# Kernel optimization log

Measured on AMD Instinct MI355X. Metric: run time of the kernel, lower is better.

The kernel has to match this reference:

```python
import jax, jax.numpy as jnp
import numpy as np

N_NODES = 10000
N_EDGES = 120000
F_IN = 66
HEADS = 10
F_HEAD = 66          # GATConv(66, 66, heads=10) -> concat 660
GCN_OUT = F_IN * HEADS * 2  # 1320


def leaky(x, slope):
    return jnp.where(x >= 0, x, slope * x)


def add_self_loops(edge_index, n):
    loops = jnp.arange(n, dtype=edge_index.dtype)
    src = jnp.concatenate([edge_index[0], loops])
    dst = jnp.concatenate([edge_index[1], loops])
    return src, dst


def gat_conv(x, src, dst, W, att_src, att_dst, bias, n):
    # x: [N, F_IN]; W: [F_IN, HEADS*F_HEAD]
    xt = (x @ W).reshape(n, HEADS, F_HEAD)
    a_s = jnp.sum(xt * att_src, axis=-1)   # [N, H]
    a_d = jnp.sum(xt * att_dst, axis=-1)   # [N, H]
    e = leaky(a_s[src] + a_d[dst], 0.2)    # [E, H]
    # segment softmax over destination nodes
    m = jax.ops.segment_max(e, dst, num_segments=n)
    m = jnp.where(jnp.isfinite(m), m, 0.0)
    ex = jnp.exp(e - m[dst])
    s = jax.ops.segment_sum(ex, dst, num_segments=n)
    alpha = ex / jnp.maximum(s[dst], 1e-16)        # [E, H]
    msg = xt[src] * alpha[:, :, None]              # [E, H, F_HEAD]
    out = jax.ops.segment_sum(msg, dst, num_segments=n)
    return out.reshape(n, HEADS * F_HEAD) + bias


def gcn_conv(x, src, dst, W, b, n):
    xt = x @ W                                     # [N, GCN_OUT]
    ones = jnp.ones(src.shape[0], dtype=xt.dtype)
    deg = jax.ops.segment_sum(ones, dst, num_segments=n)
    dinv = jax.lax.rsqrt(jnp.maximum(deg, 1.0))
    norm = dinv[src] * dinv[dst]                   # [E]
    out = jax.ops.segment_sum(xt[src] * norm[:, None], dst, num_segments=n)
    return out + b


def setup_inputs() -> dict:
    key = jax.random.key(0)
    ks = jax.random.split(key, 16)
    x = jax.random.normal(ks[0], (N_NODES, F_IN), dtype=jnp.float32)
    edge_index = jax.random.randint(ks[1], (2, N_EDGES), 0, N_NODES, dtype=jnp.int32)
    sc = 0.05
    p = {
        'x': x,
        'edge_index': edge_index,
        'W_gat': jax.random.normal(ks[2], (F_IN, HEADS * F_HEAD)) * sc,
        'att_src': jax.random.normal(ks[3], (HEADS, F_HEAD)) * sc,
        'att_dst': jax.random.normal(ks[4], (HEADS, F_HEAD)) * sc,
        'b_gat': jnp.zeros((HEADS * F_HEAD,), jnp.float32),
        'W_gcn': jax.random.normal(ks[5], (HEADS * F_HEAD, GCN_OUT)) * sc,
        'b_gcn': jnp.zeros((GCN_OUT,), jnp.float32),
        'W_g1': jax.random.normal(ks[6], (GCN_OUT, 1000)) * sc,
        'b_g1': jnp.zeros((1000,), jnp.float32),
        'W_g2': jax.random.normal(ks[7], (1000, 64)) * sc,
        'b_g2': jnp.zeros((64,), jnp.float32),
        'W_fc1': jax.random.normal(ks[8], (64, 32)) * sc,
        'b_fc1': jnp.zeros((32,), jnp.float32),
        'W_fc2': jax.random.normal(ks[9], (32, 16)) * sc,
        'b_fc2': jnp.zeros((16,), jnp.float32),
        'W_out': jax.random.normal(ks[10], (16, 1)) * sc,
        'b_out': jnp.zeros((1,), jnp.float32),
    }
    return p


def reference(x, edge_index, W_gat, att_src, att_dst, b_gat, W_gcn, b_gcn,
              W_g1, b_g1, W_g2, b_g2, W_fc1, b_fc1, W_fc2, b_fc2, W_out, b_out):
    n = x.shape[0]
    src, dst = add_self_loops(edge_index, n)
    h = gat_conv(x, src, dst, W_gat, att_src, att_dst, b_gat, n)
    h = leaky(h, 0.01)
    h = gcn_conv(h, src, dst, W_gcn, b_gcn, n)
    h = leaky(h, 0.01)
    h = leaky(h @ W_g1 + b_g1, 0.01)   # dropout = identity (eval)
    h = h @ W_g2 + b_g2
    h = leaky(h, 0.01)
    h = leaky(h @ W_fc1 + b_fc1, 0.01)
    h = leaky(h @ W_fc2 + b_fc2, 0.01)
    return h @ W_out + b_out
```

## Files before the change

kernel.cpp:

```cpp
#include <hip/hip_runtime.h>
#include <hip/hip_bf16.h>
#include <math.h>

#define N_NODES 10000
#define MPAD    10112
#define N_EDGESI 120000
#define E_TOT   130000
#define F_INPUT 66
#define HEADS   10
#define F_HEAD  66
#define F_GAT   660
#define F_GCN   1320
#define F_G1    1000
#define F_G2    64

typedef _Float16 half_t;
typedef __attribute__((ext_vector_type(4))) _Float16 f16x4;
typedef __attribute__((ext_vector_type(8))) _Float16 f16x8;
typedef __attribute__((ext_vector_type(4))) float f32x4;

#define KP_GAT 128
#define NP_GAT 768
#define KP_GCN 704
#define NP_GCN 1408
#define KP_G1  1344
#define NP_G1  1024
#define KP_G2  1024
#define NP_G2  128

__device__ __forceinline__ float lky(float x, float s){ return x >= 0.f ? x : s*x; }

#if defined(__has_builtin)
#if __has_builtin(__builtin_amdgcn_global_load_lds)
#define HAVE_GLL 1
#endif
#endif

#ifdef HAVE_GLL
#define LDSLOAD16(g, l) __builtin_amdgcn_global_load_lds( \
    (const __attribute__((address_space(1))) void*)(g),   \
    (__attribute__((address_space(3))) void*)(l), 16, 0, 0)
#else
#define LDSLOAD16(g, l) (*(f16x8*)(l) = *(const f16x8*)(g))
#endif


__global__ void k_count(const int* __restrict__ ei, int* __restrict__ counts){
    int e = blockIdx.x*256 + threadIdx.x;
    if (e >= E_TOT) return;
    int dst = (e < N_EDGESI) ? ei[N_EDGESI + e] : (e - N_EDGESI);
    atomicAdd(&counts[dst], 1);
}

__global__ void k_scan(const int* __restrict__ counts, int* __restrict__ offsets){
    __shared__ int sh[256];
    int carry = 0;
    for (int base = 0; base < N_NODES; base += 256){
        int i = base + threadIdx.x;
        int v = (i < N_NODES) ? counts[i] : 0;
        sh[threadIdx.x] = v;
        __syncthreads();
        for (int off = 1; off < 256; off <<= 1){
            int t = (threadIdx.x >= off) ? sh[threadIdx.x - off] : 0;
            __syncthreads();
            sh[threadIdx.x] += t;
            __syncthreads();
        }
        if (i < N_NODES) offsets[i] = carry + sh[threadIdx.x] - v;
        int tot = sh[255];
        __syncthreads();
        carry += tot;
    }
    if (threadIdx.x == 0) offsets[N_NODES] = carry;
}

__global__ void k_fill(const int* __restrict__ ei, const int* __restrict__ offsets,
                       int* __restrict__ cursor, int* __restrict__ src_sorted){
    int e = blockIdx.x*256 + threadIdx.x;
    if (e >= E_TOT) return;
    int s, d;
    if (e < N_EDGESI){ s = ei[e]; d = ei[N_EDGESI + e]; }
    else { s = e - N_EDGESI; d = s; }
    int pos = offsets[d] + atomicAdd(&cursor[d], 1);
    src_sorted[pos] = s;
}


__global__ void k_xh(const float* __restrict__ x, half_t* __restrict__ xh){
    int idx = blockIdx.x*256 + threadIdx.x;
    if (idx >= MPAD*KP_GAT) return;
    int r = idx >> 7, c = idx & 127;
    float v = (r < N_NODES && c < F_INPUT) ? x[r*F_INPUT + c] : 0.f;
    xh[idx] = (half_t)v;
}

__global__ void k_wt(const float* __restrict__ W, half_t* __restrict__ WT,
                     int K, int N, int Kp, int Np){
    int idx = blockIdx.x*256 + threadIdx.x;
    if (idx >= Np*Kp) return;
    int n = idx / Kp, k = idx - n*Kp;
    float v = (n < N && k < K) ? W[(size_t)k*N + n] : 0.f;
    WT[idx] = (half_t)v;
}

__global__ __launch_bounds__(256)
void k_hgemm(const half_t* __restrict__ A, const half_t* __restrict__ Bt,
             half_t* __restrict__ C, const float* __restrict__ bias,
             int Nreal, int ldc, int Kp, float slope){
    __shared__ half_t As[128*64];
    __shared__ half_t Bs[128*64];
    const int tid = threadIdx.x;
    const int l = tid & 63;
    const int wid = tid >> 6;
    const int wr = wid >> 1, wc = wid & 1;
    const int brow = blockIdx.y * 128;
    const int bcol = blockIdx.x * 128;

    f32x4 acc[4][4] = {};

    for (int k0 = 0; k0 < Kp; k0 += 64){
        #pragma unroll
        for (int i = 0; i < 4; i++){
            int s = tid + i*256;
            int row = s >> 3, chp = s & 7;
            int ch = chp ^ (row & 7);
            LDSLOAD16(A  + (size_t)(brow+row)*Kp + k0 + ch*8, &As[s*8]);
            LDSLOAD16(Bt + (size_t)(bcol+row)*Kp + k0 + ch*8, &Bs[s*8]);
        }
        __syncthreads();
        #pragma unroll
        for (int t = 0; t < 2; t++){
            f16x8 af[4], bf[4];
            #pragma unroll
            for (int m = 0; m < 4; m++){
                int row = wr*64 + m*16 + (l & 15);
                int ch = (t*4 + (l >> 4)) ^ (row & 7);
                af[m] = *(const f16x8*)&As[row*64 + ch*8];
            }
            #pragma unroll
            for (int n = 0; n < 4; n++){
                int row = wc*64 + n*16 + (l & 15);
                int ch = (t*4 + (l >> 4)) ^ (row & 7);
                bf[n] = *(const f16x8*)&Bs[row*64 + ch*8];
            }
            #pragma unroll
            for (int m = 0; m < 4; m++)
                #pragma unroll
                for (int n = 0; n < 4; n++)
                    acc[m][n] = __builtin_amdgcn_mfma_f32_16x16x32_f16(
                        af[m], bf[n], acc[m][n], 0, 0, 0);
        }
        __syncthreads();
    }

    #pragma unroll
    for (int m = 0; m < 4; m++){
        #pragma unroll
        for (int n = 0; n < 4; n++){
            int col = bcol + wc*64 + n*16 + (l & 15);
            if (col >= ldc) continue;
            float bv = (bias && col < Nreal) ? bias[col] : 0.f;
            #pragma unroll
            for (int r = 0; r < 4; r++){
                int rowg = brow + wr*64 + m*16 + ((l >> 4) << 2) + r;
                float v = (col < Nreal) ? acc[m][n][r] + bv : 0.f;
                v = (v >= 0.f) ? v : slope*v;
                C[(size_t)rowg*ldc + col] = (half_t)v;
            }
        }
    }
}


__global__ void k_attn_ad(const half_t* __restrict__ xt,
                          const float* __restrict__ att_src, const float* __restrict__ att_dst,
                          float* __restrict__ a_s, float* __restrict__ a_d){
    int t = blockIdx.x*256 + threadIdx.x;
    if (t >= N_NODES*HEADS) return;
    int n = t / HEADS, h = t - (t/HEADS)*HEADS;
    const half_t* xr = xt + (size_t)n*NP_GAT + h*F_HEAD;
    const float* as = att_src + h*F_HEAD;
    const float* ad = att_dst + h*F_HEAD;
    float s = 0.f, d = 0.f;
    for (int f = 0; f < F_HEAD; f++){ float v = (float)xr[f]; s += v*as[f]; d += v*ad[f]; }
    a_s[t] = s; a_d[t] = d;
}

__global__ void k_softmax(const int* __restrict__ offsets, const int* __restrict__ src_sorted,
                          const float* __restrict__ a_s, const float* __restrict__ a_d,
                          float* __restrict__ e_sorted, float* __restrict__ inv_s){
    int t = blockIdx.x*256 + threadIdx.x;
    if (t >= N_NODES*HEADS) return;
    int n = t / HEADS, h = t - (t/HEADS)*HEADS;
    int b = offsets[n], e = offsets[n+1];
    float ad_n = a_d[t - h + h];
    ad_n = a_d[t];
    float m = -INFINITY;
    for (int s = b; s < e; s++){
        float v = lky(a_s[src_sorted[s]*HEADS + h] + ad_n, 0.2f);
        e_sorted[(size_t)s*HEADS + h] = v;
        m = fmaxf(m, v);
    }
    float sum = 0.f;
    for (int s = b; s < e; s++){
        float ex = __expf(e_sorted[(size_t)s*HEADS + h] - m);
        e_sorted[(size_t)s*HEADS + h] = ex;
        sum += ex;
    }
    inv_s[t] = 1.0f / fmaxf(sum, 1e-16f);
}

__global__ __launch_bounds__(192)
void k_gat_agg(const int* __restrict__ offsets, const int* __restrict__ src_sorted,
               const float* __restrict__ e_sorted, const float* __restrict__ inv_s,
               const half_t* __restrict__ xt, const float* __restrict__ b_gat,
               half_t* __restrict__ out){
    int n = blockIdx.x, t = threadIdx.x;
    int f0 = 4*t;
    int h0 = min(f0/F_HEAD, HEADS-1);
    int h1 = min((f0+1)/F_HEAD, HEADS-1);
    int h2 = min((f0+2)/F_HEAD, HEADS-1);
    int h3 = min((f0+3)/F_HEAD, HEADS-1);
    int b = offsets[n], e = offsets[n+1];
    float a0=0.f, a1=0.f, a2=0.f, a3=0.f;
    int s = b;
    for (; s + 2 <= e; s += 2){
        int s0 = src_sorted[s], s1 = src_sorted[s+1];
        f16x4 v0 = *(const f16x4*)(xt + (size_t)s0*NP_GAT + f0);
        f16x4 v1 = *(const f16x4*)(xt + (size_t)s1*NP_GAT + f0);
        const float* e0 = e_sorted + (size_t)s*HEADS;
        const float* e1 = e0 + HEADS;
        a0 += e0[h0]*(float)v0.x + e1[h0]*(float)v1.x;
        a1 += e0[h1]*(float)v0.y + e1[h1]*(float)v1.y;
        a2 += e0[h2]*(float)v0.z + e1[h2]*(float)v1.z;
        a3 += e0[h3]*(float)v0.w + e1[h3]*(float)v1.w;
    }
    if (s < e){
        int s0 = src_sorted[s];
        f16x4 v0 = *(const f16x4*)(xt + (size_t)s0*NP_GAT + f0);
        const float* e0 = e_sorted + (size_t)s*HEADS;
        a0 += e0[h0]*(float)v0.x;
        a1 += e0[h1]*(float)v0.y;
        a2 += e0[h2]*(float)v0.z;
        a3 += e0[h3]*(float)v0.w;
    }
    if (f0 >= KP_GCN) return;
    half_t* orow = out + (size_t)n*KP_GCN + f0;
    if (f0 < F_GAT){
        const float* iv = inv_s + n*HEADS;
        f16x4 r;
        r.x = (half_t)lky(a0*iv[h0] + b_gat[f0  ], 0.01f);
        r.y = (half_t)lky(a1*iv[h1] + b_gat[f0+1], 0.01f);
        r.z = (half_t)lky(a2*iv[h2] + b_gat[f0+2], 0.01f);
        r.w = (half_t)lky(a3*iv[h3] + b_gat[f0+3], 0.01f);
        *(f16x4*)orow = r;
    } else {
        f16x4 z = {(half_t)0.f,(half_t)0.f,(half_t)0.f,(half_t)0.f};
        *(f16x4*)orow = z;
    }
}


__global__ void k_dinv(const int* __restrict__ offsets, float* __restrict__ dinv){
    int n = blockIdx.x*256 + threadIdx.x;
    if (n >= N_NODES) return;
    float deg = (float)(offsets[n+1] - offsets[n]);
    dinv[n] = rsqrtf(fmaxf(deg, 1.0f));
}

__global__ __launch_bounds__(192)
void k_gcn_pre(const int* __restrict__ offsets, const int* __restrict__ src_sorted,
               const float* __restrict__ dinv, const half_t* __restrict__ h1,
               half_t* __restrict__ agg){
    int n = blockIdx.x, t = threadIdx.x;
    if (t >= 176) return;
    int f0 = 4*t;
    int b = offsets[n], e = offsets[n+1];
    float a0=0.f, a1=0.f, a2=0.f, a3=0.f;
    int s = b;
    for (; s + 2 <= e; s += 2){
        int s0 = src_sorted[s], s1 = src_sorted[s+1];
        float n0 = dinv[s0], n1 = dinv[s1];
        f16x4 v0 = *(const f16x4*)(h1 + (size_t)s0*KP_GCN + f0);
        f16x4 v1 = *(const f16x4*)(h1 + (size_t)s1*KP_GCN + f0);
        a0 += n0*(float)v0.x + n1*(float)v1.x;
        a1 += n0*(float)v0.y + n1*(float)v1.y;
        a2 += n0*(float)v0.z + n1*(float)v1.z;
        a3 += n0*(float)v0.w + n1*(float)v1.w;
    }
    if (s < e){
        int s0 = src_sorted[s];
        float n0 = dinv[s0];
        f16x4 v0 = *(const f16x4*)(h1 + (size_t)s0*KP_GCN + f0);
        a0 += n0*(float)v0.x;
        a1 += n0*(float)v0.y;
        a2 += n0*(float)v0.z;
        a3 += n0*(float)v0.w;
    }
    float dn = dinv[n];
    f16x4 r;
    r.x = (half_t)(dn*a0); r.y = (half_t)(dn*a1);
    r.z = (half_t)(dn*a2); r.w = (half_t)(dn*a3);
    *(f16x4*)(agg + (size_t)n*KP_GCN + f0) = r;
}

__global__ __launch_bounds__(256)
void k_tail(const half_t* __restrict__ h4,
            const float* __restrict__ Wfc1, const float* __restrict__ bfc1,
            const float* __restrict__ Wfc2, const float* __restrict__ bfc2,
            const float* __restrict__ Wout, const float* __restrict__ bout,
            float* __restrict__ out){
    __shared__ float W1[64*32];
    __shared__ float W2[32*16];
    __shared__ float Wo[16];
    __shared__ float b1[32];
    __shared__ float b2[16];
    __shared__ float r1[8][32];
    __shared__ float r2[8][16];
    int tid = threadIdx.x;
    for (int i = tid; i < 64*32; i += 256) W1[i] = Wfc1[i];
    for (int i = tid; i < 32*16; i += 256) W2[i] = Wfc2[i];
    if (tid < 16) Wo[tid] = Wout[tid];
    if (tid < 32) b1[tid] = bfc1[tid];
    if (tid < 16) b2[tid] = bfc2[tid];
    __syncthreads();
    int g = tid >> 5, j = tid & 31;
    int node = blockIdx.x*8 + g;
    const half_t* hr = h4 + (size_t)node*F_G2;
    float acc = 0.f;
    #pragma unroll 8
    for (int i = 0; i < 64; i++) acc += (float)hr[i]*W1[i*32 + j];
    r1[g][j] = lky(acc + b1[j], 0.01f);
    __syncthreads();
    if (j < 16){
        float a2 = 0.f;
        #pragma unroll
        for (int i = 0; i < 32; i++) a2 += r1[g][i]*W2[i*16 + j];
        r2[g][j] = lky(a2 + b2[j], 0.01f);
    }
    __syncthreads();
    if (j == 0){
        float a3 = 0.f;
        #pragma unroll
        for (int i = 0; i < 16; i++) a3 += r2[g][i]*Wo[i];
        out[node] = a3 + bout[0];
    }
}


extern "C" void kernel_launch(void* const* d_in, const int* in_sizes, int n_in,
                              void* d_out, int out_size, void* d_ws, size_t ws_size,
                              hipStream_t stream){
    const float* x       = (const float*)d_in[0];
    const int*   ei      = (const int*)  d_in[1];
    const float* W_gat   = (const float*)d_in[2];
    const float* att_src = (const float*)d_in[3];
    const float* att_dst = (const float*)d_in[4];
    const float* b_gat   = (const float*)d_in[5];
    const float* W_gcn   = (const float*)d_in[6];
    const float* b_gcn   = (const float*)d_in[7];
    const float* W_g1    = (const float*)d_in[8];
    const float* b_g1    = (const float*)d_in[9];
    const float* W_g2    = (const float*)d_in[10];
    const float* b_g2    = (const float*)d_in[11];
    const float* W_fc1   = (const float*)d_in[12];
    const float* b_fc1   = (const float*)d_in[13];
    const float* W_fc2   = (const float*)d_in[14];
    const float* b_fc2   = (const float*)d_in[15];
    const float* W_out   = (const float*)d_in[16];
    const float* b_out   = (const float*)d_in[17];
    float* out = (float*)d_out;
    char* ws = (char*)d_ws;

    size_t off = 0;
    auto alloc = [&](size_t bytes){ size_t o = off; off += (bytes + 255) & ~(size_t)255; return o; };
    size_t o_counts = alloc(N_NODES*4);
    size_t o_cursor = alloc(N_NODES*4);
    size_t o_offs   = alloc((N_NODES+1)*4);
    size_t o_as     = alloc(N_NODES*HEADS*4);
    size_t o_ad     = alloc(N_NODES*HEADS*4);
    size_t o_invs   = alloc(N_NODES*HEADS*4);
    size_t o_dinv   = alloc(N_NODES*4);
    size_t o_srcs   = alloc(E_TOT*4);
    size_t o_esrt   = alloc((size_t)E_TOT*HEADS*4);
    size_t o_xh     = alloc((size_t)MPAD*KP_GAT*2);
    size_t o_xt     = alloc((size_t)MPAD*NP_GAT*2);
    size_t o_h1     = alloc((size_t)N_NODES*KP_GCN*2);
    size_t o_agg    = alloc((size_t)MPAD*KP_GCN*2);
    size_t o_h2     = alloc((size_t)MPAD*KP_G1*2);
    size_t o_h3     = alloc((size_t)MPAD*KP_G2*2);
    size_t o_h4     = alloc((size_t)MPAD*F_G2*2);
    size_t o_wgatT  = alloc((size_t)NP_GAT*KP_GAT*2);
    size_t o_wgcnT  = alloc((size_t)NP_GCN*KP_GCN*2);
    size_t o_wg1T   = alloc((size_t)NP_G1*KP_G1*2);
    size_t o_wg2T   = alloc((size_t)NP_G2*KP_G2*2);

    int*    counts  = (int*)(ws + o_counts);
    int*    cursor  = (int*)(ws + o_cursor);
    int*    offsets = (int*)(ws + o_offs);
    float*  a_s     = (float*)(ws + o_as);
    float*  a_d     = (float*)(ws + o_ad);
    float*  inv_s   = (float*)(ws + o_invs);
    float*  dinv    = (float*)(ws + o_dinv);
    int*    src_srt = (int*)(ws + o_srcs);
    float*  e_srt   = (float*)(ws + o_esrt);
    half_t* xh      = (half_t*)(ws + o_xh);
    half_t* xt_h    = (half_t*)(ws + o_xt);
    half_t* h1h     = (half_t*)(ws + o_h1);
    half_t* aggh    = (half_t*)(ws + o_agg);
    half_t* h2h     = (half_t*)(ws + o_h2);
    half_t* h3h     = (half_t*)(ws + o_h3);
    half_t* h4h     = (half_t*)(ws + o_h4);
    half_t* WgatT   = (half_t*)(ws + o_wgatT);
    half_t* WgcnT   = (half_t*)(ws + o_wgcnT);
    half_t* Wg1T    = (half_t*)(ws + o_wg1T);
    half_t* Wg2T    = (half_t*)(ws + o_wg2T);

    hipMemsetAsync(counts, 0, N_NODES*4, stream);
    hipMemsetAsync(cursor, 0, N_NODES*4, stream);
    k_count<<<(E_TOT+255)/256, 256, 0, stream>>>(ei, counts);
    k_scan<<<1, 256, 0, stream>>>(counts, offsets);
    k_fill<<<(E_TOT+255)/256, 256, 0, stream>>>(ei, offsets, cursor, src_srt);
    k_dinv<<<(N_NODES+255)/256, 256, 0, stream>>>(offsets, dinv);

    k_xh<<<(MPAD*KP_GAT+255)/256, 256, 0, stream>>>(x, xh);
    k_wt<<<(NP_GAT*KP_GAT+255)/256, 256, 0, stream>>>(W_gat, WgatT, F_INPUT, F_GAT, KP_GAT, NP_GAT);
    k_wt<<<(NP_GCN*KP_GCN+255)/256, 256, 0, stream>>>(W_gcn, WgcnT, F_GAT, F_GCN, KP_GCN, NP_GCN);
    k_wt<<<(NP_G1*KP_G1+255)/256, 256, 0, stream>>>(W_g1, Wg1T, F_GCN, F_G1, KP_G1, NP_G1);
    k_wt<<<(NP_G2*KP_G2+255)/256, 256, 0, stream>>>(W_g2, Wg2T, F_G1, F_G2, KP_G2, NP_G2);

    k_hgemm<<<dim3(NP_GAT/128, MPAD/128), 256, 0, stream>>>(
        xh, WgatT, xt_h, nullptr, F_GAT, NP_GAT, KP_GAT, 1.0f);
    k_attn_ad<<<(N_NODES*HEADS+255)/256, 256, 0, stream>>>(xt_h, att_src, att_dst, a_s, a_d);
    k_softmax<<<(N_NODES*HEADS+255)/256, 256, 0, stream>>>(offsets, src_srt, a_s, a_d, e_srt, inv_s);
    k_gat_agg<<<N_NODES, 192, 0, stream>>>(offsets, src_srt, e_srt, inv_s, xt_h, b_gat, h1h);

    k_gcn_pre<<<N_NODES, 192, 0, stream>>>(offsets, src_srt, dinv, h1h, aggh);
    k_hgemm<<<dim3(NP_GCN/128, MPAD/128), 256, 0, stream>>>(
        aggh, WgcnT, h2h, b_gcn, F_GCN, KP_G1, KP_GCN, 0.01f);

    k_hgemm<<<dim3(NP_G1/128, MPAD/128), 256, 0, stream>>>(
        h2h, Wg1T, h3h, b_g1, F_G1, KP_G2, KP_G1, 0.01f);
    k_hgemm<<<dim3(NP_G2/128, MPAD/128), 256, 0, stream>>>(
        h3h, Wg2T, h4h, b_g2, F_G2, F_G2, KP_G2, 0.01f);
    k_tail<<<N_NODES/8, 256, 0, stream>>>(h4h, W_fc1, b_fc1, W_fc2, b_fc2,
                                          W_out, b_out, out);
}
```

Baseline: 386.0 us.

## Remap GEMM workgroups per XCD and unroll gather loops by four

The GEMM kernel now remaps its linear workgroup id so that neighbouring output tiles are placed on the same XCD, which should improve L2 reuse of the A and B panels on MI355X's multi-die layout. The GAT and GCN aggregation loops are unrolled from two to four neighbours per iteration, so more independent gather loads are in flight at once. The attention-coefficient kernel reads pairs of half values with unrolled loops, and a redundant a_d load is removed. The costs are higher register pressure in the aggregation kernels and a more complex tile-index computation.

```diff
diff --git a/kernel.cpp b/kernel.cpp
--- a/kernel.cpp
+++ b/kernel.cpp
@@ -15,6 +15,7 @@
 #define F_G2    64
 
 typedef _Float16 half_t;
+typedef __attribute__((ext_vector_type(2))) _Float16 f16x2;
 typedef __attribute__((ext_vector_type(4))) _Float16 f16x4;
 typedef __attribute__((ext_vector_type(8))) _Float16 f16x8;
 typedef __attribute__((ext_vector_type(4))) float f32x4;
@@ -113,8 +114,17 @@
     const int l = tid & 63;
     const int wid = tid >> 6;
     const int wr = wid >> 1, wc = wid & 1;
-    const int brow = blockIdx.y * 128;
-    const int bcol = blockIdx.x * 128;
+
+    const int gx = gridDim.x;
+    const int nwg = gx * gridDim.y;
+    const int orig = blockIdx.y * gx + blockIdx.x;
+    const int q = nwg >> 3, r8 = nwg & 7;
+    const int xcd = orig & 7, lin = orig >> 3;
+    const int wgid = (xcd < r8 ? xcd*(q+1) : r8*(q+1) + (xcd-r8)*q) + lin;
+    const int bx = wgid % gx, by = wgid / gx;
+
+    const int brow = by * 128;
+    const int bcol = bx * 128;
 
     f32x4 acc[4][4] = {};
 
@@ -182,7 +192,13 @@
     const float* as = att_src + h*F_HEAD;
     const float* ad = att_dst + h*F_HEAD;
     float s = 0.f, d = 0.f;
-    for (int f = 0; f < F_HEAD; f++){ float v = (float)xr[f]; s += v*as[f]; d += v*ad[f]; }
+    #pragma unroll
+    for (int f = 0; f < F_HEAD; f += 2){
+        f16x2 v = *(const f16x2*)(xr + f);
+        float vx = (float)v.x, vy = (float)v.y;
+        s += vx*as[f] + vy*as[f+1];
+        d += vx*ad[f] + vy*ad[f+1];
+    }
     a_s[t] = s; a_d[t] = d;
 }
 
@@ -193,8 +209,7 @@
     if (t >= N_NODES*HEADS) return;
     int n = t / HEADS, h = t - (t/HEADS)*HEADS;
     int b = offsets[n], e = offsets[n+1];
-    float ad_n = a_d[t - h + h];
-    ad_n = a_d[t];
+    float ad_n = a_d[t];
     float m = -INFINITY;
     for (int s = b; s < e; s++){
         float v = lky(a_s[src_sorted[s]*HEADS + h] + ad_n, 0.2f);
@@ -224,18 +239,23 @@
     int b = offsets[n], e = offsets[n+1];
     float a0=0.f, a1=0.f, a2=0.f, a3=0.f;
     int s = b;
-    for (; s + 2 <= e; s += 2){
-        int s0 = src_sorted[s], s1 = src_sorted[s+1];
+    for (; s + 4 <= e; s += 4){
+        int s0 = src_sorted[s],   s1 = src_sorted[s+1];
+        int s2 = src_sorted[s+2], s3 = src_sorted[s+3];
         f16x4 v0 = *(const f16x4*)(xt + (size_t)s0*NP_GAT + f0);
         f16x4 v1 = *(const f16x4*)(xt + (size_t)s1*NP_GAT + f0);
+        f16x4 v2 = *(const f16x4*)(xt + (size_t)s2*NP_GAT + f0);
+        f16x4 v3 = *(const f16x4*)(xt + (size_t)s3*NP_GAT + f0);
         const float* e0 = e_sorted + (size_t)s*HEADS;
         const float* e1 = e0 + HEADS;
-        a0 += e0[h0]*(float)v0.x + e1[h0]*(float)v1.x;
-        a1 += e0[h1]*(float)v0.y + e1[h1]*(float)v1.y;
-        a2 += e0[h2]*(float)v0.z + e1[h2]*(float)v1.z;
-        a3 += e0[h3]*(float)v0.w + e1[h3]*(float)v1.w;
-    }
-    if (s < e){
+        const float* e2 = e0 + 2*HEADS;
+        const float* e3 = e0 + 3*HEADS;
+        a0 += e0[h0]*(float)v0.x + e1[h0]*(float)v1.x + e2[h0]*(float)v2.x + e3[h0]*(float)v3.x;
+        a1 += e0[h1]*(float)v0.y + e1[h1]*(float)v1.y + e2[h1]*(float)v2.y + e3[h1]*(float)v3.y;
+        a2 += e0[h2]*(float)v0.z + e1[h2]*(float)v1.z + e2[h2]*(float)v2.z + e3[h2]*(float)v3.z;
+        a3 += e0[h3]*(float)v0.w + e1[h3]*(float)v1.w + e2[h3]*(float)v2.w + e3[h3]*(float)v3.w;
+    }
+    for (; s < e; s++){
         int s0 = src_sorted[s];
         f16x4 v0 = *(const f16x4*)(xt + (size_t)s0*NP_GAT + f0);
         const float* e0 = e_sorted + (size_t)s*HEADS;
@@ -278,17 +298,20 @@
     int b = offsets[n], e = offsets[n+1];
     float a0=0.f, a1=0.f, a2=0.f, a3=0.f;
     int s = b;
-    for (; s + 2 <= e; s += 2){
-        int s0 = src_sorted[s], s1 = src_sorted[s+1];
-        float n0 = dinv[s0], n1 = dinv[s1];
+    for (; s + 4 <= e; s += 4){
+        int s0 = src_sorted[s],   s1 = src_sorted[s+1];
+        int s2 = src_sorted[s+2], s3 = src_sorted[s+3];
+        float n0 = dinv[s0], n1 = dinv[s1], n2 = dinv[s2], n3 = dinv[s3];
         f16x4 v0 = *(const f16x4*)(h1 + (size_t)s0*KP_GCN + f0);
         f16x4 v1 = *(const f16x4*)(h1 + (size_t)s1*KP_GCN + f0);
-        a0 += n0*(float)v0.x + n1*(float)v1.x;
-        a1 += n0*(float)v0.y + n1*(float)v1.y;
-        a2 += n0*(float)v0.z + n1*(float)v1.z;
-        a3 += n0*(float)v0.w + n1*(float)v1.w;
-    }
-    if (s < e){
+        f16x4 v2 = *(const f16x4*)(h1 + (size_t)s2*KP_GCN + f0);
+        f16x4 v3 = *(const f16x4*)(h1 + (size_t)s3*KP_GCN + f0);
+        a0 += n0*(float)v0.x + n1*(float)v1.x + n2*(float)v2.x + n3*(float)v3.x;
+        a1 += n0*(float)v0.y + n1*(float)v1.y + n2*(float)v2.y + n3*(float)v3.y;
+        a2 += n0*(float)v0.z + n1*(float)v1.z + n2*(float)v2.z + n3*(float)v3.z;
+        a3 += n0*(float)v0.w + n1*(float)v1.w + n2*(float)v2.w + n3*(float)v3.w;
+    }
+    for (; s < e; s++){
         int s0 = src_sorted[s];
         float n0 = dinv[s0];
         f16x4 v0 = *(const f16x4*)(h1 + (size_t)s0*KP_GCN + f0);
```

Result: no change. 380.7 us (-1.4%).
